# Optimization experiments

Hardware: AMD Instinct MI355X
Metric: run time of the kernel (lower is better)

## Reference

```python
import jax, jax.numpy as jnp
import numpy as np

NEG_INF = -1e30  # large negative instead of float('-inf') for fp16/bf16 safety in softmax


def setup_inputs() -> dict:
    key = jax.random.key(0)
    k1, k2, k3, k4 = jax.random.split(key, 4)
    B, T, C, H = 8, 2048, 768, 64
    x = jax.random.normal(k1, (B, T, C), dtype=jnp.float32)
    # nn.Linear(n_embd, head_size, bias=False): y = x @ W.T, W shape (head_size, n_embd)
    s = 1.0 / np.sqrt(C)
    Wk = jax.random.uniform(k2, (H, C), dtype=jnp.float32, minval=-s, maxval=s)
    Wq = jax.random.uniform(k3, (H, C), dtype=jnp.float32, minval=-s, maxval=s)
    Wv = jax.random.uniform(k4, (H, C), dtype=jnp.float32, minval=-s, maxval=s)
    return {"x": x, "Wk": Wk, "Wq": Wq, "Wv": Wv}


def reference(x, Wk, Wq, Wv):
    # x: [B,T,C]; Wk/Wq/Wv: [H,C]
    k = jnp.einsum('btc,hc->bth', x, Wk)  # [B,T,H]
    q = jnp.einsum('btc,hc->bth', x, Wq)
    v = jnp.einsum('btc,hc->bth', x, Wv)
    att = jnp.einsum('bqh,bkh->bqk', q, k)  # [B,T,T], NOTE: no 1/sqrt(H) scaling, faithful to source
    T = x.shape[1]
    causal = jnp.tril(jnp.ones((T, T), dtype=bool))
    att = jnp.where(causal, att, NEG_INF)
    att = jax.nn.softmax(att, axis=-1)
    out = jnp.einsum('bqk,bkh->bqh', att, v)  # [B,T,H]
    return out
```

## Files before the change

kernel.cpp:

```cpp
#include <hip/hip_runtime.h>
#include <hip/hip_bf16.h>
#include <stdint.h>

typedef float    f32x4  __attribute__((ext_vector_type(4)));
typedef float    f32x16 __attribute__((ext_vector_type(16)));
typedef short    s16x8  __attribute__((ext_vector_type(8)));
typedef uint32_t u32x4  __attribute__((ext_vector_type(4)));
typedef uint32_t u32x2  __attribute__((ext_vector_type(2)));

#define NB 8
#define NT 2048
#define NC 768
#define NH 64
#define LOG2E 1.4426950408889634f

__device__ __forceinline__ uint32_t f2bf1(float f) {
  union { float f; uint32_t u; } v; v.f = f;
  uint32_t u = v.u;
  return (u + 0x7fffu + ((u >> 16) & 1u)) >> 16;
}
__device__ __forceinline__ uint32_t packbf2(float lo, float hi) {
  union { __hip_bfloat162 h; uint32_t u; } c;
  c.h = __float22bfloat162_rn(float2{lo, hi});
  return c.u;
}
__device__ __forceinline__ float bf2f(short s) {
  union { float f; uint32_t u; } v; v.u = ((uint32_t)(uint16_t)s) << 16; return v.f;
}

__global__ __launch_bounds__(256) void wconv_kernel(
    const float* __restrict__ Wk, const float* __restrict__ Wq,
    const float* __restrict__ Wv, short* __restrict__ Wf)
{
  int f = blockIdx.x * 256 + threadIdx.x;
  int lane = f & 63;
  int rest = f >> 6;
  int ks = rest % 48;
  int nt = rest / 48;
  int col = lane & 31, half = lane >> 5;
  int n = nt * 32 + col;
  int k = ks * 16 + half * 8;
  const float* src;
  float sc = 1.0f;
  if (n < 64)       { src = Wq + (size_t)n * NC + k; sc = LOG2E; }
  else if (n < 128) { src = Wk + (size_t)(n - 64) * NC + k; }
  else              { src = Wv + (size_t)(n - 128) * NC + k; }
  f32x4 a = *(const f32x4*)src;
  f32x4 b = *(const f32x4*)(src + 4);
  u32x4 o = {packbf2(a[0] * sc, a[1] * sc), packbf2(a[2] * sc, a[3] * sc),
             packbf2(b[0] * sc, b[1] * sc), packbf2(b[2] * sc, b[3] * sc)};
  *(u32x4*)&Wf[(size_t)f * 8] = o;
}

__global__ __launch_bounds__(384, 2) void proj_kernel(
    const float* __restrict__ x, const short* __restrict__ Wf,
    short* __restrict__ qfb, short* __restrict__ kfb, short* __restrict__ vfb)
{
  __shared__ short ldsX[32 * 768];

  const int tid  = threadIdx.x;
  const int lane = tid & 63;
  const int w    = tid >> 6;
  const int col  = lane & 31;
  const int half = lane >> 5;
  const int tg   = blockIdx.x;
  const int t0   = tg * 32;

  {
#pragma unroll
    for (int i = 0; i < 8; ++i) {
      int c   = tid + 384 * i;
      int tok = c / 96, g = c % 96;
      const float* src = x + (size_t)(t0 + tok) * NC + g * 8;
      f32x4 a = *(const f32x4*)src;
      f32x4 d = *(const f32x4*)(src + 4);
      int swz = (g & ~7) | ((g ^ tok) & 7);
      u32x4 o = {packbf2(a[0], a[1]), packbf2(a[2], a[3]),
                 packbf2(d[0], d[1]), packbf2(d[2], d[3])};
      *(u32x4*)&ldsX[tok * 768 + swz * 8] = o;
    }
  }
  __syncthreads();

  f32x16 acc;
#pragma unroll
  for (int e = 0; e < 16; ++e) acc[e] = 0.f;

  const short* wbase = Wf + (((size_t)w * 48) << 9) + lane * 8;
  auto loadW = [&](int ks) -> s16x8 { return *(const s16x8*)(wbase + ((size_t)ks << 9)); };
  auto loadA = [&](int ks) -> s16x8 {
    int grp = ks * 2 + half;
    int swz = (grp & ~7) | ((grp ^ col) & 7);
    return *(const s16x8*)&ldsX[col * 768 + swz * 8];
  };
  {
    s16x8 wA = loadW(0), aA = loadA(0), wB, aB;
#pragma unroll
    for (int ks = 0; ks < 48; ks += 2) {
      wB = loadW(ks + 1); aB = loadA(ks + 1);
      acc = __builtin_amdgcn_mfma_f32_32x32x16_bf16(aA, wA, acc, 0, 0, 0);
      if (ks + 2 < 48) { wA = loadW(ks + 2); aA = loadA(ks + 2); }
      acc = __builtin_amdgcn_mfma_f32_32x32x16_bf16(aB, wB, acc, 0, 0, 0);
    }
  }
  __syncthreads();

  short* scr = ldsX + w * 1088;
  const size_t base = (size_t)tg * 2048;
  if (w < 4) {
#pragma unroll
    for (int r = 0; r < 16; ++r) {
      int rd = (r & 3) + 8 * (r >> 2) + 4 * half;
      scr[rd * 34 + col] = (short)f2bf1(acc[r]);
    }
    short* dst = (w < 2) ? qfb : kfb;
    int ksBase = (w & 1) * 2;
#pragma unroll
    for (int j = 0; j < 2; ++j) {
      s16x8 v = *(const s16x8*)&scr[col * 34 + j * 16 + half * 8];
      *(s16x8*)&dst[base + (ksBase + j) * 512 + lane * 8] = v;
    }
  } else {
#pragma unroll
    for (int r = 0; r < 16; ++r) {
      int rd = (r & 3) + 8 * (r >> 2) + 4 * half;
      scr[col * 34 + rd] = (short)f2bf1(acc[r]);
    }
    int hh = w - 4;
#pragma unroll
    for (int j = 0; j < 2; ++j) {
      s16x8 v = *(const s16x8*)&scr[col * 34 + j * 16 + half * 8];
      *(s16x8*)&vfb[base + (hh * 2 + j) * 512 + lane * 8] = v;
    }
  }
}

__global__ __launch_bounds__(512, 2) void attn_kernel(
    const short* __restrict__ qfb, const short* __restrict__ kfb,
    const short* __restrict__ vfb, float* __restrict__ out)
{
  __shared__ short ldsOb[8 * 32 * 72];
  __shared__ float ldsL[8 * 32];

  const int tid  = threadIdx.x;
  const int lane = tid & 63;
  const int w8   = tid >> 6;
  const int col  = lane & 31;
  const int half = lane >> 5;
  const int b    = blockIdx.x & 7;
  const int p    = blockIdx.x >> 3;

  const short* kfp = kfb + (size_t)b * 64 * 2048 + lane * 8;
  const short* vfp = vfb + (size_t)b * 64 * 2048 + lane * 8;

#pragma unroll 1
  for (int iter = 0; iter < 2; ++iter) {
    const int qt = iter ? p : 63 - p;
    const int nT = qt + 1;

    s16x8 qf[4];
    {
      const short* qp = qfb + (size_t)(b * 64 + qt) * 2048 + lane * 8;
#pragma unroll
      for (int ks = 0; ks < 4; ++ks) qf[ks] = *(const s16x8*)(qp + ks * 512);
    }

    f32x16 oacc[2];
#pragma unroll
    for (int i = 0; i < 2; ++i)
#pragma unroll
      for (int e = 0; e < 16; ++e) oacc[i][e] = 0.f;
    float l = 0.f;

    s16x8 kA[4], vA[4], kB[4], vB[4];
    auto loadT = [&](s16x8* dk, s16x8* dv, int t) {
      const short* kp = kfp + (size_t)t * 2048;
      const short* vp = vfp + (size_t)t * 2048;
#pragma unroll
      for (int i = 0; i < 4; ++i) {
        dk[i] = *(const s16x8*)(kp + i * 512);
        dv[i] = *(const s16x8*)(vp + i * 512);
      }
    };
    auto body = [&](s16x8* ck, s16x8* cv, int t) {
      f32x16 s;
#pragma unroll
      for (int e = 0; e < 16; ++e) s[e] = 0.f;
      __builtin_amdgcn_s_setprio(1);
#pragma unroll
      for (int ks = 0; ks < 4; ++ks)
        s = __builtin_amdgcn_mfma_f32_32x32x16_bf16(ck[ks], qf[ks], s, 0, 0, 0);
      __builtin_amdgcn_s_setprio(0);

      if (t == qt) {
#pragma unroll
        for (int r = 0; r < 16; ++r) {
          int rd = (r & 3) + 8 * (r >> 2) + 4 * half;
          if (rd > col) s[r] = -1000.f;
        }
      }
      float pp[16];
      float rs = 0.f;
#pragma unroll
      for (int r = 0; r < 16; ++r) { pp[r] = exp2f(s[r]); rs += pp[r]; }
      rs += __shfl_xor(rs, 32);
      l += rs;

      uint32_t pw[8];
#pragma unroll
      for (int i = 0; i < 8; ++i) pw[i] = packbf2(pp[2 * i], pp[2 * i + 1]);
#pragma unroll
      for (int kc = 0; kc < 2; ++kc) {
        uint32_t s0 = half ? pw[4 * kc]     : pw[4 * kc + 2];
        uint32_t s1 = half ? pw[4 * kc + 1] : pw[4 * kc + 3];
        uint32_t r0 = __shfl_xor(s0, 32);
        uint32_t r1 = __shfl_xor(s1, 32);
        uint32_t w0 = half ? r0 : pw[4 * kc];
        uint32_t w1 = half ? r1 : pw[4 * kc + 1];
        uint32_t w2 = half ? pw[4 * kc + 2] : r0;
        uint32_t w3 = half ? pw[4 * kc + 3] : r1;
        union { u32x4 u; s16x8 v; } pf;
        pf.u = (u32x4){w0, w1, w2, w3};
        __builtin_amdgcn_s_setprio(1);
#pragma unroll
        for (int ht = 0; ht < 2; ++ht)
          oacc[ht] = __builtin_amdgcn_mfma_f32_32x32x16_bf16(cv[ht * 2 + kc], pf.v, oacc[ht], 0, 0, 0);
        __builtin_amdgcn_s_setprio(0);
      }
    };

    int t = w8;
    if (t < nT) loadT(kA, vA, t);
    if (t + 8 < nT) loadT(kB, vB, t + 8);
    for (; t + 8 < nT; t += 16) {
      body(kA, vA, t);
      if (t + 16 < nT) loadT(kA, vA, t + 16);
      body(kB, vB, t + 8);
      if (t + 24 < nT) loadT(kB, vB, t + 24);
    }
    if (t < nT) body(kA, vA, t);

    if (half == 0) ldsL[w8 * 32 + col] = l;
#pragma unroll
    for (int ht = 0; ht < 2; ++ht)
#pragma unroll
      for (int u = 0; u < 4; ++u) {
        int h = ht * 32 + 8 * u + 4 * half;
        u32x2 pk = {packbf2(oacc[ht][4 * u + 0], oacc[ht][4 * u + 1]),
                    packbf2(oacc[ht][4 * u + 2], oacc[ht][4 * u + 3])};
        *(u32x2*)&ldsOb[(w8 * 32 + col) * 72 + h] = pk;
      }
    __syncthreads();

    {
      const int rr = tid >> 4;
      const int h0 = (tid & 15) * 4;
      float Ls = 0.f;
      float o[4] = {0.f, 0.f, 0.f, 0.f};
#pragma unroll
      for (int s = 0; s < 8; ++s) {
        Ls += ldsL[s * 32 + rr];
        const short* row = &ldsOb[(s * 32 + rr) * 72 + h0];
#pragma unroll
        for (int j = 0; j < 4; ++j) o[j] += bf2f(row[j]);
      }
      float inv = 1.0f / Ls;
      float* ob = out + (size_t)(b * NT + qt * 32 + rr) * NH + h0;
      *(f32x4*)ob = (f32x4){o[0] * inv, o[1] * inv, o[2] * inv, o[3] * inv};
    }
    __syncthreads();
  }
}

extern "C" void kernel_launch(void* const* d_in, const int* in_sizes, int n_in,
                              void* d_out, int out_size, void* d_ws, size_t ws_size,
                              hipStream_t stream) {
  const float* x  = (const float*)d_in[0];
  const float* Wk = (const float*)d_in[1];
  const float* Wq = (const float*)d_in[2];
  const float* Wv = (const float*)d_in[3];
  float* out = (float*)d_out;

  char* ws = (char*)d_ws;
  short* Wf  = (short*)(ws);
  short* qfb = (short*)(ws + (512 << 10));
  short* kfb = (short*)(ws + (512 << 10) + (2 << 20));
  short* vfb = (short*)(ws + (512 << 10) + (4 << 20));

  hipLaunchKernelGGL(wconv_kernel, dim3(72),  dim3(256), 0, stream, Wk, Wq, Wv, Wf);
  hipLaunchKernelGGL(proj_kernel,  dim3(512), dim3(384), 0, stream, x, Wf, qfb, kfb, vfb);
  hipLaunchKernelGGL(attn_kernel,  dim3(256), dim3(512), 0, stream, qfb, kfb, vfb, out);
}
```

Measured before the change: 109.2 us.

## Fuse weight conversion, projection and attention into one cooperative kernel

Merges the three launches (weight bf16 conversion, QKV projection, causal attention) into a single cooperative kernel of 256 blocks, separating the phases with grid-wide syncs. The projection phase now processes 64 tokens per block in two passes of 12 wave tasks, using a larger dynamic LDS buffer. This removes two kernel launch gaps and tail effects, at the cost of grid.sync overhead and lower parallelism in the projection phase (256 blocks instead of 512, with some waves idle).

```diff
diff --git a/kernel.cpp b/kernel.cpp
--- a/kernel.cpp
+++ b/kernel.cpp
@@ -1,6 +1,9 @@
 #include <hip/hip_runtime.h>
+#include <hip/hip_cooperative_groups.h>
 #include <hip/hip_bf16.h>
 #include <stdint.h>
+
+namespace cg = cooperative_groups;
 
 typedef float    f32x4  __attribute__((ext_vector_type(4)));
 typedef float    f32x16 __attribute__((ext_vector_type(16)));
@@ -14,6 +17,9 @@
 #define NH 64
 #define LOG2E 1.4426950408889634f
 
+#define LDS_SHORTS (64 * 768 + 8 * 1088)
+#define LDS_BYTES  (LDS_SHORTS * 2)
+
 __device__ __forceinline__ uint32_t f2bf1(float f) {
   union { float f; uint32_t u; } v; v.f = f;
   uint32_t u = v.u;
@@ -28,247 +34,245 @@
   union { float f; uint32_t u; } v; v.u = ((uint32_t)(uint16_t)s) << 16; return v.f;
 }
 
-__global__ __launch_bounds__(256) void wconv_kernel(
-    const float* __restrict__ Wk, const float* __restrict__ Wq,
-    const float* __restrict__ Wv, short* __restrict__ Wf)
+__global__ __launch_bounds__(512, 2) void fused_kernel(
+    const float* __restrict__ x, const float* __restrict__ Wk,
+    const float* __restrict__ Wq, const float* __restrict__ Wv,
+    short* __restrict__ Wf, short* __restrict__ qfb,
+    short* __restrict__ kfb, short* __restrict__ vfb,
+    float* __restrict__ out)
 {
-  int f = blockIdx.x * 256 + threadIdx.x;
-  int lane = f & 63;
-  int rest = f >> 6;
-  int ks = rest % 48;
-  int nt = rest / 48;
-  int col = lane & 31, half = lane >> 5;
-  int n = nt * 32 + col;
-  int k = ks * 16 + half * 8;
-  const float* src;
-  float sc = 1.0f;
-  if (n < 64)       { src = Wq + (size_t)n * NC + k; sc = LOG2E; }
-  else if (n < 128) { src = Wk + (size_t)(n - 64) * NC + k; }
-  else              { src = Wv + (size_t)(n - 128) * NC + k; }
-  f32x4 a = *(const f32x4*)src;
-  f32x4 b = *(const f32x4*)(src + 4);
-  u32x4 o = {packbf2(a[0] * sc, a[1] * sc), packbf2(a[2] * sc, a[3] * sc),
-             packbf2(b[0] * sc, b[1] * sc), packbf2(b[2] * sc, b[3] * sc)};
-  *(u32x4*)&Wf[(size_t)f * 8] = o;
-}
-
-__global__ __launch_bounds__(384, 2) void proj_kernel(
-    const float* __restrict__ x, const short* __restrict__ Wf,
-    short* __restrict__ qfb, short* __restrict__ kfb, short* __restrict__ vfb)
-{
-  __shared__ short ldsX[32 * 768];
-
-  const int tid  = threadIdx.x;
-  const int lane = tid & 63;
-  const int w    = tid >> 6;
-  const int col  = lane & 31;
-  const int half = lane >> 5;
-  const int tg   = blockIdx.x;
-  const int t0   = tg * 32;
-
-  {
-#pragma unroll
-    for (int i = 0; i < 8; ++i) {
-      int c   = tid + 384 * i;
-      int tok = c / 96, g = c % 96;
-      const float* src = x + (size_t)(t0 + tok) * NC + g * 8;
-      f32x4 a = *(const f32x4*)src;
-      f32x4 d = *(const f32x4*)(src + 4);
-      int swz = (g & ~7) | ((g ^ tok) & 7);
-      u32x4 o = {packbf2(a[0], a[1]), packbf2(a[2], a[3]),
-                 packbf2(d[0], d[1]), packbf2(d[2], d[3])};
-      *(u32x4*)&ldsX[tok * 768 + swz * 8] = o;
-    }
-  }
-  __syncthreads();
-
-  f32x16 acc;
-#pragma unroll
-  for (int e = 0; e < 16; ++e) acc[e] = 0.f;
-
-  const short* wbase = Wf + (((size_t)w * 48) << 9) + lane * 8;
-  auto loadW = [&](int ks) -> s16x8 { return *(const s16x8*)(wbase + ((size_t)ks << 9)); };
-  auto loadA = [&](int ks) -> s16x8 {
-    int grp = ks * 2 + half;
-    int swz = (grp & ~7) | ((grp ^ col) & 7);
-    return *(const s16x8*)&ldsX[col * 768 + swz * 8];
-  };
-  {
-    s16x8 wA = loadW(0), aA = loadA(0), wB, aB;
-#pragma unroll
-    for (int ks = 0; ks < 48; ks += 2) {
-      wB = loadW(ks + 1); aB = loadA(ks + 1);
-      acc = __builtin_amdgcn_mfma_f32_32x32x16_bf16(aA, wA, acc, 0, 0, 0);
-      if (ks + 2 < 48) { wA = loadW(ks + 2); aA = loadA(ks + 2); }
-      acc = __builtin_amdgcn_mfma_f32_32x32x16_bf16(aB, wB, acc, 0, 0, 0);
-    }
-  }
-  __syncthreads();
-
-  short* scr = ldsX + w * 1088;
-  const size_t base = (size_t)tg * 2048;
-  if (w < 4) {
-#pragma unroll
-    for (int r = 0; r < 16; ++r) {
-      int rd = (r & 3) + 8 * (r >> 2) + 4 * half;
-      scr[rd * 34 + col] = (short)f2bf1(acc[r]);
-    }
-    short* dst = (w < 2) ? qfb : kfb;
-    int ksBase = (w & 1) * 2;
-#pragma unroll
-    for (int j = 0; j < 2; ++j) {
-      s16x8 v = *(const s16x8*)&scr[col * 34 + j * 16 + half * 8];
-      *(s16x8*)&dst[base + (ksBase + j) * 512 + lane * 8] = v;
-    }
-  } else {
-#pragma unroll
-    for (int r = 0; r < 16; ++r) {
-      int rd = (r & 3) + 8 * (r >> 2) + 4 * half;
-      scr[col * 34 + rd] = (short)f2bf1(acc[r]);
-    }
-    int hh = w - 4;
-#pragma unroll
-    for (int j = 0; j < 2; ++j) {
-      s16x8 v = *(const s16x8*)&scr[col * 34 + j * 16 + half * 8];
-      *(s16x8*)&vfb[base + (hh * 2 + j) * 512 + lane * 8] = v;
-    }
-  }
-}
-
-__global__ __launch_bounds__(512, 2) void attn_kernel(
-    const short* __restrict__ qfb, const short* __restrict__ kfb,
-    const short* __restrict__ vfb, float* __restrict__ out)
-{
-  __shared__ short ldsOb[8 * 32 * 72];
-  __shared__ float ldsL[8 * 32];
+  extern __shared__ short lds[];
+  cg::grid_group grid = cg::this_grid();
 
   const int tid  = threadIdx.x;
   const int lane = tid & 63;
   const int w8   = tid >> 6;
   const int col  = lane & 31;
   const int half = lane >> 5;
-  const int b    = blockIdx.x & 7;
-  const int p    = blockIdx.x >> 3;
-
-  const short* kfp = kfb + (size_t)b * 64 * 2048 + lane * 8;
-  const short* vfp = vfb + (size_t)b * 64 * 2048 + lane * 8;
-
-#pragma unroll 1
-  for (int iter = 0; iter < 2; ++iter) {
-    const int qt = iter ? p : 63 - p;
-    const int nT = qt + 1;
-
-    s16x8 qf[4];
-    {
-      const short* qp = qfb + (size_t)(b * 64 + qt) * 2048 + lane * 8;
-#pragma unroll
-      for (int ks = 0; ks < 4; ++ks) qf[ks] = *(const s16x8*)(qp + ks * 512);
+  const int blk  = blockIdx.x;
+
+  {
+    int wc = (w8 == 0) ? blk : ((w8 == 1) ? 256 + blk : 288);
+    if (wc < 288) {
+      int ks = wc % 48, nt = wc / 48;
+      int n = nt * 32 + col, k = ks * 16 + half * 8;
+      const float* src; float sc = 1.0f;
+      if (n < 64)       { src = Wq + (size_t)n * NC + k; sc = LOG2E; }
+      else if (n < 128) { src = Wk + (size_t)(n - 64) * NC + k; }
+      else              { src = Wv + (size_t)(n - 128) * NC + k; }
+      f32x4 a = *(const f32x4*)src;
+      f32x4 b = *(const f32x4*)(src + 4);
+      u32x4 o = {packbf2(a[0] * sc, a[1] * sc), packbf2(a[2] * sc, a[3] * sc),
+                 packbf2(b[0] * sc, b[1] * sc), packbf2(b[2] * sc, b[3] * sc)};
+      *(u32x4*)&Wf[((size_t)wc * 64 + lane) * 8] = o;
     }
-
-    f32x16 oacc[2];
-#pragma unroll
-    for (int i = 0; i < 2; ++i)
-#pragma unroll
-      for (int e = 0; e < 16; ++e) oacc[i][e] = 0.f;
-    float l = 0.f;
-
-    s16x8 kA[4], vA[4], kB[4], vB[4];
-    auto loadT = [&](s16x8* dk, s16x8* dv, int t) {
-      const short* kp = kfp + (size_t)t * 2048;
-      const short* vp = vfp + (size_t)t * 2048;
-#pragma unroll
-      for (int i = 0; i < 4; ++i) {
-        dk[i] = *(const s16x8*)(kp + i * 512);
-        dv[i] = *(const s16x8*)(vp + i * 512);
-      }
-    };
-    auto body = [&](s16x8* ck, s16x8* cv, int t) {
-      f32x16 s;
-#pragma unroll
-      for (int e = 0; e < 16; ++e) s[e] = 0.f;
-      __builtin_amdgcn_s_setprio(1);
-#pragma unroll
-      for (int ks = 0; ks < 4; ++ks)
-        s = __builtin_amdgcn_mfma_f32_32x32x16_bf16(ck[ks], qf[ks], s, 0, 0, 0);
-      __builtin_amdgcn_s_setprio(0);
-
-      if (t == qt) {
-#pragma unroll
-        for (int r = 0; r < 16; ++r) {
-          int rd = (r & 3) + 8 * (r >> 2) + 4 * half;
-          if (rd > col) s[r] = -1000.f;
-        }
-      }
-      float pp[16];
-      float rs = 0.f;
-#pragma unroll
-      for (int r = 0; r < 16; ++r) { pp[r] = exp2f(s[r]); rs += pp[r]; }
-      rs += __shfl_xor(rs, 32);
-      l += rs;
-
-      uint32_t pw[8];
-#pragma unroll
-      for (int i = 0; i < 8; ++i) pw[i] = packbf2(pp[2 * i], pp[2 * i + 1]);
-#pragma unroll
-      for (int kc = 0; kc < 2; ++kc) {
-        uint32_t s0 = half ? pw[4 * kc]     : pw[4 * kc + 2];
-        uint32_t s1 = half ? pw[4 * kc + 1] : pw[4 * kc + 3];
-        uint32_t r0 = __shfl_xor(s0, 32);
-        uint32_t r1 = __shfl_xor(s1, 32);
-        uint32_t w0 = half ? r0 : pw[4 * kc];
-        uint32_t w1 = half ? r1 : pw[4 * kc + 1];
-        uint32_t w2 = half ? pw[4 * kc + 2] : r0;
-        uint32_t w3 = half ? pw[4 * kc + 3] : r1;
-        union { u32x4 u; s16x8 v; } pf;
-        pf.u = (u32x4){w0, w1, w2, w3};
-        __builtin_amdgcn_s_setprio(1);
-#pragma unroll
-        for (int ht = 0; ht < 2; ++ht)
-          oacc[ht] = __builtin_amdgcn_mfma_f32_32x32x16_bf16(cv[ht * 2 + kc], pf.v, oacc[ht], 0, 0, 0);
-        __builtin_amdgcn_s_setprio(0);
-      }
-    };
-
-    int t = w8;
-    if (t < nT) loadT(kA, vA, t);
-    if (t + 8 < nT) loadT(kB, vB, t + 8);
-    for (; t + 8 < nT; t += 16) {
-      body(kA, vA, t);
-      if (t + 16 < nT) loadT(kA, vA, t + 16);
-      body(kB, vB, t + 8);
-      if (t + 24 < nT) loadT(kB, vB, t + 24);
-    }
-    if (t < nT) body(kA, vA, t);
-
-    if (half == 0) ldsL[w8 * 32 + col] = l;
-#pragma unroll
-    for (int ht = 0; ht < 2; ++ht)
-#pragma unroll
-      for (int u = 0; u < 4; ++u) {
-        int h = ht * 32 + 8 * u + 4 * half;
-        u32x2 pk = {packbf2(oacc[ht][4 * u + 0], oacc[ht][4 * u + 1]),
-                    packbf2(oacc[ht][4 * u + 2], oacc[ht][4 * u + 3])};
-        *(u32x2*)&ldsOb[(w8 * 32 + col) * 72 + h] = pk;
-      }
-    __syncthreads();
-
-    {
-      const int rr = tid >> 4;
-      const int h0 = (tid & 15) * 4;
-      float Ls = 0.f;
-      float o[4] = {0.f, 0.f, 0.f, 0.f};
-#pragma unroll
-      for (int s = 0; s < 8; ++s) {
-        Ls += ldsL[s * 32 + rr];
-        const short* row = &ldsOb[(s * 32 + rr) * 72 + h0];
-#pragma unroll
-        for (int j = 0; j < 4; ++j) o[j] += bf2f(row[j]);
-      }
-      float inv = 1.0f / Ls;
-      float* ob = out + (size_t)(b * NT + qt * 32 + rr) * NH + h0;
-      *(f32x4*)ob = (f32x4){o[0] * inv, o[1] * inv, o[2] * inv, o[3] * inv};
+  }
+  __threadfence();
+  grid.sync();
+
+  {
+    const int t0 = blk * 64;
+#pragma unroll
+    for (int i = 0; i < 12; ++i) {
+      int c = tid + 512 * i;
+      int tok = c / 96, g = c % 96;
+      const float* src = x + (size_t)(t0 + tok) * NC + g * 8;
+      f32x4 a = *(const f32x4*)src;
+      f32x4 d = *(const f32x4*)(src + 4);
+      int swz = (g & ~7) | ((g ^ (tok & 31)) & 7);
+      u32x4 o = {packbf2(a[0], a[1]), packbf2(a[2], a[3]),
+                 packbf2(d[0], d[1]), packbf2(d[2], d[3])};
+      *(u32x4*)&lds[tok * 768 + swz * 8] = o;
     }
     __syncthreads();
+
+    short* scr = lds + 64 * 768 + w8 * 1088;
+#pragma unroll 1
+    for (int pass = 0; pass < 2; ++pass) {
+      int task = pass ? (8 + w8) : w8;
+      if (task < 12) {
+        int tt = (task >= 6) ? 1 : 0;
+        int n  = task - tt * 6;
+        const short* ldsXb = lds + tt * 24576;
+        f32x16 acc;
+#pragma unroll
+        for (int e = 0; e < 16; ++e) acc[e] = 0.f;
+        const short* wbase = Wf + (((size_t)n * 48) << 9) + lane * 8;
+        {
+          auto loadW = [&](int ks) -> s16x8 { return *(const s16x8*)(wbase + ((size_t)ks << 9)); };
+          auto loadA = [&](int ks) -> s16x8 {
+            int grp = ks * 2 + half;
+            int swz = (grp & ~7) | ((grp ^ col) & 7);
+            return *(const s16x8*)&ldsXb[col * 768 + swz * 8];
+          };
+          s16x8 wA = loadW(0), aA = loadA(0), wB, aB;
+#pragma unroll
+          for (int ks = 0; ks < 48; ks += 2) {
+            wB = loadW(ks + 1); aB = loadA(ks + 1);
+            acc = __builtin_amdgcn_mfma_f32_32x32x16_bf16(aA, wA, acc, 0, 0, 0);
+            if (ks + 2 < 48) { wA = loadW(ks + 2); aA = loadA(ks + 2); }
+            acc = __builtin_amdgcn_mfma_f32_32x32x16_bf16(aB, wB, acc, 0, 0, 0);
+          }
+        }
+        const size_t base = (size_t)(blk * 2 + tt) * 2048;
+        if (n < 4) {
+#pragma unroll
+          for (int r = 0; r < 16; ++r) {
+            int rd = (r & 3) + 8 * (r >> 2) + 4 * half;
+            scr[rd * 34 + col] = (short)f2bf1(acc[r]);
+          }
+          short* dst = (n < 2) ? qfb : kfb;
+          int ksBase = (n & 1) * 2;
+#pragma unroll
+          for (int j = 0; j < 2; ++j) {
+            s16x8 v = *(const s16x8*)&scr[col * 34 + j * 16 + half * 8];
+            *(s16x8*)&dst[base + (ksBase + j) * 512 + lane * 8] = v;
+          }
+        } else {
+#pragma unroll
+          for (int r = 0; r < 16; ++r) {
+            int rd = (r & 3) + 8 * (r >> 2) + 4 * half;
+            scr[col * 34 + rd] = (short)f2bf1(acc[r]);
+          }
+          int hh = n - 4;
+#pragma unroll
+          for (int j = 0; j < 2; ++j) {
+            s16x8 v = *(const s16x8*)&scr[col * 34 + j * 16 + half * 8];
+            *(s16x8*)&vfb[base + (hh * 2 + j) * 512 + lane * 8] = v;
+          }
+        }
+      }
+    }
+  }
+  __threadfence();
+  grid.sync();
+
+  {
+    short* ldsOb = lds;
+    float* ldsL  = (float*)(lds + 8 * 32 * 72);
+    const int b = blk & 7;
+    const int p = blk >> 3;
+
+    const short* kfp = kfb + (size_t)b * 64 * 2048 + lane * 8;
+    const short* vfp = vfb + (size_t)b * 64 * 2048 + lane * 8;
+
+#pragma unroll 1
+    for (int iter = 0; iter < 2; ++iter) {
+      const int qt = iter ? p : 63 - p;
+      const int nT = qt + 1;
+
+      s16x8 qf[4];
+      {
+        const short* qp = qfb + (size_t)(b * 64 + qt) * 2048 + lane * 8;
+#pragma unroll
+        for (int ks = 0; ks < 4; ++ks) qf[ks] = *(const s16x8*)(qp + ks * 512);
+      }
+
+      f32x16 oacc[2];
+#pragma unroll
+      for (int i = 0; i < 2; ++i)
+#pragma unroll
+        for (int e = 0; e < 16; ++e) oacc[i][e] = 0.f;
+      float l = 0.f;
+
+      s16x8 kA[4], vA[4], kB[4], vB[4];
+      auto loadT = [&](s16x8* dk, s16x8* dv, int t) {
+        const short* kp = kfp + (size_t)t * 2048;
+        const short* vp = vfp + (size_t)t * 2048;
+#pragma unroll
+        for (int i = 0; i < 4; ++i) {
+          dk[i] = *(const s16x8*)(kp + i * 512);
+          dv[i] = *(const s16x8*)(vp + i * 512);
+        }
+      };
+      auto body = [&](s16x8* ck, s16x8* cv, int t) {
+        f32x16 s;
+#pragma unroll
+        for (int e = 0; e < 16; ++e) s[e] = 0.f;
+        __builtin_amdgcn_s_setprio(1);
+#pragma unroll
+        for (int ks = 0; ks < 4; ++ks)
+          s = __builtin_amdgcn_mfma_f32_32x32x16_bf16(ck[ks], qf[ks], s, 0, 0, 0);
+        __builtin_amdgcn_s_setprio(0);
+
+        if (t == qt) {
+#pragma unroll
+          for (int r = 0; r < 16; ++r) {
+            int rd = (r & 3) + 8 * (r >> 2) + 4 * half;
+            if (rd > col) s[r] = -1000.f;
+          }
+        }
+        float pp[16];
+        float rs = 0.f;
+#pragma unroll
+        for (int r = 0; r < 16; ++r) { pp[r] = exp2f(s[r]); rs += pp[r]; }
+        rs += __shfl_xor(rs, 32);
+        l += rs;
+
+        uint32_t pw[8];
+#pragma unroll
+        for (int i = 0; i < 8; ++i) pw[i] = packbf2(pp[2 * i], pp[2 * i + 1]);
+#pragma unroll
+        for (int kc = 0; kc < 2; ++kc) {
+          uint32_t s0 = half ? pw[4 * kc]     : pw[4 * kc + 2];
+          uint32_t s1 = half ? pw[4 * kc + 1] : pw[4 * kc + 3];
+          uint32_t r0 = __shfl_xor(s0, 32);
+          uint32_t r1 = __shfl_xor(s1, 32);
+          uint32_t w0 = half ? r0 : pw[4 * kc];
+          uint32_t w1 = half ? r1 : pw[4 * kc + 1];
+          uint32_t w2 = half ? pw[4 * kc + 2] : r0;
+          uint32_t w3 = half ? pw[4 * kc + 3] : r1;
+          union { u32x4 u; s16x8 v; } pf;
+          pf.u = (u32x4){w0, w1, w2, w3};
+          __builtin_amdgcn_s_setprio(1);
+#pragma unroll
+          for (int ht = 0; ht < 2; ++ht)
+            oacc[ht] = __builtin_amdgcn_mfma_f32_32x32x16_bf16(cv[ht * 2 + kc], pf.v, oacc[ht], 0, 0, 0);
+          __builtin_amdgcn_s_setprio(0);
+        }
+      };
+
+      int t = w8;
+      if (t < nT) loadT(kA, vA, t);
+      if (t + 8 < nT) loadT(kB, vB, t + 8);
+      for (; t + 8 < nT; t += 16) {
+        body(kA, vA, t);
+        if (t + 16 < nT) loadT(kA, vA, t + 16);
+        body(kB, vB, t + 8);
+        if (t + 24 < nT) loadT(kB, vB, t + 24);
+      }
+      if (t < nT) body(kA, vA, t);
+
+      if (half == 0) ldsL[w8 * 32 + col] = l;
+#pragma unroll
+      for (int ht = 0; ht < 2; ++ht)
+#pragma unroll
+        for (int u = 0; u < 4; ++u) {
+          int h = ht * 32 + 8 * u + 4 * half;
+          u32x2 pk = {packbf2(oacc[ht][4 * u + 0], oacc[ht][4 * u + 1]),
+                      packbf2(oacc[ht][4 * u + 2], oacc[ht][4 * u + 3])};
+          *(u32x2*)&ldsOb[(w8 * 32 + col) * 72 + h] = pk;
+        }
+      __syncthreads();
+
+      {
+        const int rr = tid >> 4;
+        const int h0 = (tid & 15) * 4;
+        float Ls = 0.f;
+        float o[4] = {0.f, 0.f, 0.f, 0.f};
+#pragma unroll
+        for (int s = 0; s < 8; ++s) {
+          Ls += ldsL[s * 32 + rr];
+          const short* row = &ldsOb[(s * 32 + rr) * 72 + h0];
+#pragma unroll
+          for (int j = 0; j < 4; ++j) o[j] += bf2f(row[j]);
+        }
+        float inv = 1.0f / Ls;
+        float* ob = out + (size_t)(b * NT + qt * 32 + rr) * NH + h0;
+        *(f32x4*)ob = (f32x4){o[0] * inv, o[1] * inv, o[2] * inv, o[3] * inv};
+      }
+      __syncthreads();
+    }
   }
 }
 
@@ -287,7 +291,11 @@
   short* kfb = (short*)(ws + (512 << 10) + (2 << 20));
   short* vfb = (short*)(ws + (512 << 10) + (4 << 20));
 
-  hipLaunchKernelGGL(wconv_kernel, dim3(72),  dim3(256), 0, stream, Wk, Wq, Wv, Wf);
-  hipLaunchKernelGGL(proj_kernel,  dim3(512), dim3(384), 0, stream, x, Wf, qfb, kfb, vfb);
-  hipLaunchKernelGGL(attn_kernel,  dim3(256), dim3(512), 0, stream, qfb, kfb, vfb, out);
-}
+  hipFuncSetAttribute((const void*)fused_kernel,
+                      hipFuncAttributeMaxDynamicSharedMemorySize, LDS_BYTES);
+
+  void* args[] = {(void*)&x, (void*)&Wk, (void*)&Wq, (void*)&Wv,
+                  (void*)&Wf, (void*)&qfb, (void*)&kfb, (void*)&vfb, (void*)&out};
+  hipLaunchCooperativeKernel((const void*)fused_kernel, dim3(256), dim3(512),
+                             args, (unsigned int)LDS_BYTES, stream);
+}
```

Result: slower. 265.0 us (+142.7%).
